# Kernel tuning notes

Hardware: AMD Instinct MI355X
Metric: run time of the kernel (lower is better)

Reference implementation:

```python
import jax, jax.numpy as jnp
import numpy as np

D = 2048      # token_dim (forced equal to visual feat dim by concat shapes)
V = 10000     # vocab size
B = 32        # batch
X = 36        # regions
T = 20        # max_len / caption length
FEAT = 2048


def setup_inputs() -> dict:
    key = jax.random.key(0)
    ks = jax.random.split(key, 20)
    s = 0.02
    inp = {
        "features": jax.random.normal(ks[0], (B, X, FEAT), jnp.float32),
        "caption": jax.random.randint(ks[1], (B, T), 0, V),
        "emb": jax.random.normal(ks[2], (V, D), jnp.float32) * s,
        # attention LSTMCell: input 3*D, hidden D
        "Wih_a": jax.random.normal(ks[3], (4 * D, 3 * D), jnp.float32) * s,
        "Whh_a": jax.random.normal(ks[4], (4 * D, D), jnp.float32) * s,
        "bih_a": jnp.zeros((4 * D,), jnp.float32),
        "bhh_a": jnp.zeros((4 * D,), jnp.float32),
        # language LSTMCell: input 2*D, hidden D
        "Wih_l": jax.random.normal(ks[5], (4 * D, 2 * D), jnp.float32) * s,
        "Whh_l": jax.random.normal(ks[6], (4 * D, D), jnp.float32) * s,
        "bih_l": jnp.zeros((4 * D,), jnp.float32),
        "bhh_l": jnp.zeros((4 * D,), jnp.float32),
        # attention MLP
        "Wv": jax.random.normal(ks[7], (D, FEAT), jnp.float32) * s,
        "bv": jnp.zeros((D,), jnp.float32),
        "Wh": jax.random.normal(ks[8], (D, D), jnp.float32) * s,
        "bh": jnp.zeros((D,), jnp.float32),
        "Wa": jax.random.normal(ks[9], (1, D), jnp.float32) * s,
        "ba": jnp.zeros((1,), jnp.float32),
        # output projection
        "Wfc": jax.random.normal(ks[10], (V, D), jnp.float32) * s,
        "bfc": jnp.zeros((V,), jnp.float32),
    }
    return inp


def _lstm_cell(x, h, c, Wih, Whh, bih, bhh):
    # PyTorch LSTMCell: gates in (i, f, g, o) order
    z = x @ Wih.T + bih + h @ Whh.T + bhh
    i, f, g, o = jnp.split(z, 4, axis=-1)
    c_new = jax.nn.sigmoid(f) * c + jax.nn.sigmoid(i) * jnp.tanh(g)
    h_new = jax.nn.sigmoid(o) * jnp.tanh(c_new)
    return h_new, c_new


def reference(features, caption, emb, Wih_a, Whh_a, bih_a, bhh_a,
              Wih_l, Whh_l, bih_l, bhh_l, Wv, bv, Wh, bh, Wa, ba, Wfc, bfc):
    v_bar = jnp.mean(features, axis=1)            # [B, 2048]
    embs = emb[caption]                            # [B, T, D]
    a_v = features @ Wv.T + bv                     # [B, X, D], t-invariant

    h0 = jnp.zeros((features.shape[0], D), features.dtype)
    carry0 = (h0, h0, h0, h0)  # (h_attn, c_attn, h_lang, c_lang)

    def step(carry, e_t):
        h_a, c_a, h_l, c_l = carry
        x = jnp.concatenate([h_l, v_bar, e_t], axis=1)          # [B, 3D]
        h_a, c_a = _lstm_cell(x, h_a, c_a, Wih_a, Whh_a, bih_a, bhh_a)
        # additive attention (NB: softmax over trailing singleton dim,
        # reproduced faithfully from the source -> weights are all ones)
        a_h = (h_a @ Wh.T + bh)[:, None, :]                      # [B, 1, D]
        a = jnp.tanh(a_v + a_h) @ Wa.T + ba                      # [B, X, 1]
        a_w = jax.nn.softmax(a, axis=-1)                         # [B, X, 1]
        v_hat = jnp.sum(a_w * features, axis=1)                  # [B, 2048]
        x2 = jnp.concatenate([h_a, v_hat], axis=1)               # [B, 2D]
        h_l, c_l = _lstm_cell(x2, h_l, c_l, Wih_l, Whh_l, bih_l, bhh_l)
        logits_t = h_l @ Wfc.T + bfc                             # [B, V]
        return (h_a, c_a, h_l, c_l), logits_t

    _, logits = jax.lax.scan(step, carry0, jnp.swapaxes(embs, 0, 1))  # [T, B, V]
    logits = jnp.swapaxes(logits, 0, 1)                               # [B, T, V]
    return jax.nn.log_softmax(logits, axis=2)
```

## Files before the change

kernel.cpp:

```cpp
#include <hip/hip_runtime.h>

typedef unsigned short u16;
typedef __attribute__((ext_vector_type(8))) short bf16x8;
typedef __attribute__((ext_vector_type(4))) float f32x4;

#define DD 2048
#define VV 10000
#define BB 32
#define TT 20

__device__ __forceinline__ u16 f2bf(float f) {
    unsigned u = __float_as_uint(f);
    u += 0x7fffu + ((u >> 16) & 1u);
    return (u16)(u >> 16);
}
__device__ __forceinline__ float bf2f(u16 h) {
    return __uint_as_float(((unsigned)h) << 16);
}

__global__ __launch_bounds__(256) void cast_weights(
    const float* __restrict__ Wih_a, const float* __restrict__ Whh_a,
    const float* __restrict__ Wih_l, const float* __restrict__ Whh_l,
    const float* __restrict__ Wfc,
    u16* __restrict__ Wcat_a, u16* __restrict__ Wcat_l, u16* __restrict__ Wfc_b)
{
    const long long S1 = 8192LL * 4096;
    const long long S3 = 20480000LL;
    long long g = (long long)blockIdx.x * 256 + threadIdx.x;
    long long e = g * 4;
    const float* src;
    u16* dst;
    if (e < S1) {
        int n = (int)(e >> 12), k = (int)(e & 4095);
        src = (k < 2048) ? (Wih_a + (size_t)n * 6144 + k)
                         : (Whh_a + (size_t)n * 2048 + (k - 2048));
        dst = Wcat_a + e;
    } else if (e < 2 * S1) {
        long long e2 = e - S1;
        int n = (int)(e2 >> 12), k = (int)(e2 & 4095);
        src = (k < 2048) ? (Wih_l + (size_t)n * 4096 + k)
                         : (Whh_l + (size_t)n * 2048 + (k - 2048));
        dst = Wcat_l + e2;
    } else {
        long long e3 = e - 2 * S1;
        if (e3 >= S3) return;
        src = Wfc + e3;
        dst = Wfc_b + e3;
    }
    float4 v = *(const float4*)src;
    ushort4 o;
    o.x = f2bf(v.x); o.y = f2bf(v.y); o.z = f2bf(v.z); o.w = f2bf(v.w);
    *(ushort4*)dst = o;
}

__global__ __launch_bounds__(256) void prep(
    const float* __restrict__ features,
    u16* __restrict__ vbar, u16* __restrict__ vhat,
    float* __restrict__ c_a, float* __restrict__ c_l,
    u16* __restrict__ Ha0, u16* __restrict__ Hl0)
{
    int i = blockIdx.x * 256 + threadIdx.x;
    int b = i >> 11, d = i & 2047;
    const float* f = features + (size_t)b * 36 * 2048 + d;
    float s = 0.f;
#pragma unroll
    for (int x = 0; x < 36; ++x) s += f[(size_t)x * 2048];
    vhat[i] = f2bf(s);
    vbar[i] = f2bf(s * (1.f / 36.f));
    c_a[i] = 0.f; c_l[i] = 0.f;
    Ha0[i] = 0;  Hl0[i] = 0;
}

__global__ __launch_bounds__(256) void embed_k(
    const float* __restrict__ emb, const int* __restrict__ caption,
    u16* __restrict__ embs)
{
    int i = blockIdx.x * 256 + threadIdx.x;
    int m = i >> 11, d = i & 2047;
    int t = m >> 5, b = m & 31;
    int tok = caption[b * TT + t];
    embs[i] = f2bf(emb[(size_t)tok * 2048 + d]);
}

template <int MT>
__global__ __launch_bounds__(256) void pre_gemm(
    const u16* __restrict__ A, const float* __restrict__ W,
    int ldw, int kofs,
    const float* __restrict__ bias0, const float* __restrict__ bias1,
    const float* __restrict__ addend, float* __restrict__ out)
{
    const int lane = threadIdx.x & 63;
    const int wv = threadIdx.x >> 6;
    const int lr = lane & 15, lq = lane >> 4;
    const int n0 = blockIdx.x * 64 + wv * 16;
    const int m0 = blockIdx.y * (MT * 16);

    f32x4 acc[MT];
#pragma unroll
    for (int i = 0; i < MT; ++i) acc[i] = (f32x4){0.f, 0.f, 0.f, 0.f};

    const float* wrow = W + (size_t)(n0 + lr) * ldw + kofs + lq * 8;
    const u16* arow = A + (size_t)(m0 + lr) * 2048 + lq * 8;

    for (int k = 0; k < 2048; k += 32) {
        float4 wlo = *(const float4*)(wrow + k);
        float4 whi = *(const float4*)(wrow + k + 4);
        bf16x8 bf;
        bf[0] = (short)f2bf(wlo.x); bf[1] = (short)f2bf(wlo.y);
        bf[2] = (short)f2bf(wlo.z); bf[3] = (short)f2bf(wlo.w);
        bf[4] = (short)f2bf(whi.x); bf[5] = (short)f2bf(whi.y);
        bf[6] = (short)f2bf(whi.z); bf[7] = (short)f2bf(whi.w);
#pragma unroll
        for (int mt = 0; mt < MT; ++mt) {
            bf16x8 af = *(const bf16x8*)(arow + (size_t)mt * 16 * 2048 + k);
            acc[mt] = __builtin_amdgcn_mfma_f32_16x16x32_bf16(af, bf, acc[mt], 0, 0, 0);
        }
    }
    const int n = n0 + lr;
    float badd = 0.f;
    if (bias0) badd += bias0[n];
    if (bias1) badd += bias1[n];
#pragma unroll
    for (int mt = 0; mt < MT; ++mt) {
#pragma unroll
        for (int r = 0; r < 4; ++r) {
            int m = m0 + mt * 16 + lq * 4 + r;
            float v = acc[mt][r] + badd;
            if (addend) v += addend[(size_t)(m & 31) * 8192 + n];
            out[(size_t)m * 8192 + n] = v;
        }
    }
}

__global__ __launch_bounds__(512) void step_kernel(
    const u16* __restrict__ A0, const u16* __restrict__ A1,
    const u16* __restrict__ W, const float* __restrict__ zconst,
    float* __restrict__ c, u16* __restrict__ hout)
{
    __shared__ float zred[4][32][64];
    const int lane = threadIdx.x & 63;
    const int w = threadIdx.x >> 6;
    const int lr = lane & 15, lq = lane >> 4;
    const int d0 = blockIdx.x * 16;

    const u16* Aptr = (w < 4) ? A0 : A1;
    const int kA = (w & 3) * 512 + lq * 8;
    const int kW = w * 512 + lq * 8;

    f32x4 acc[2][4];
#pragma unroll
    for (int m = 0; m < 2; ++m)
#pragma unroll
        for (int g = 0; g < 4; ++g) acc[m][g] = (f32x4){0.f, 0.f, 0.f, 0.f};

    const u16* a_row0 = Aptr + (size_t)lr * 2048 + kA;
    const u16* a_row1 = Aptr + (size_t)(16 + lr) * 2048 + kA;
    const u16* b_row[4];
#pragma unroll
    for (int g = 0; g < 4; ++g)
        b_row[g] = W + (size_t)(g * 2048 + d0 + lr) * 4096 + kW;

    for (int kk = 0; kk < 512; kk += 32) {
        bf16x8 a0 = *(const bf16x8*)(a_row0 + kk);
        bf16x8 a1 = *(const bf16x8*)(a_row1 + kk);
#pragma unroll
        for (int g = 0; g < 4; ++g) {
            bf16x8 bf = *(const bf16x8*)(b_row[g] + kk);
            acc[0][g] = __builtin_amdgcn_mfma_f32_16x16x32_bf16(a0, bf, acc[0][g], 0, 0, 0);
            acc[1][g] = __builtin_amdgcn_mfma_f32_16x16x32_bf16(a1, bf, acc[1][g], 0, 0, 0);
        }
    }

    if (w >= 4) {
#pragma unroll
        for (int m = 0; m < 2; ++m)
#pragma unroll
            for (int g = 0; g < 4; ++g)
#pragma unroll
                for (int r = 0; r < 4; ++r)
                    zred[w - 4][m * 16 + lq * 4 + r][g * 16 + lr] = acc[m][g][r];
    }
    __syncthreads();
    if (w < 4) {
#pragma unroll
        for (int m = 0; m < 2; ++m)
#pragma unroll
            for (int g = 0; g < 4; ++g)
#pragma unroll
                for (int r = 0; r < 4; ++r)
                    zred[w][m * 16 + lq * 4 + r][g * 16 + lr] += acc[m][g][r];
    }
    __syncthreads();

    const int b = threadIdx.x >> 4;
    const int j = threadIdx.x & 15;
    const int d = d0 + j;
    float z[4];
#pragma unroll
    for (int g = 0; g < 4; ++g) {
        float s = zconst[(size_t)b * 8192 + g * 2048 + d];
#pragma unroll
        for (int wv = 0; wv < 4; ++wv) s += zred[wv][b][g * 16 + j];
        z[g] = s;
    }
    float ig = 1.f / (1.f + __expf(-z[0]));
    float fg = 1.f / (1.f + __expf(-z[1]));
    float gg = tanhf(z[2]);
    float og = 1.f / (1.f + __expf(-z[3]));
    float cn = fg * c[(size_t)b * 2048 + d] + ig * gg;
    c[(size_t)b * 2048 + d] = cn;
    hout[(size_t)b * 2048 + d] = f2bf(og * tanhf(cn));
}

template <int MT>
__global__ __launch_bounds__(256) void logits_gemm(
    const u16* __restrict__ A, const u16* __restrict__ Wb,
    const float* __restrict__ bias, float* __restrict__ out)
{
    const int lane = threadIdx.x & 63;
    const int wv = threadIdx.x >> 6;
    const int lr = lane & 15, lq = lane >> 4;
    const int n0 = blockIdx.x * 64 + wv * 16;
    if (n0 >= VV) return;
    const int m0 = blockIdx.y * (MT * 16);

    f32x4 acc[MT];
#pragma unroll
    for (int i = 0; i < MT; ++i) acc[i] = (f32x4){0.f, 0.f, 0.f, 0.f};

    const u16* wrow = Wb + (size_t)(n0 + lr) * 2048 + lq * 8;
    const u16* arow = A + (size_t)(m0 + lr) * 2048 + lq * 8;

    for (int k = 0; k < 2048; k += 32) {
        bf16x8 bf = *(const bf16x8*)(wrow + k);
#pragma unroll
        for (int mt = 0; mt < MT; ++mt) {
            bf16x8 af = *(const bf16x8*)(arow + (size_t)mt * 16 * 2048 + k);
            acc[mt] = __builtin_amdgcn_mfma_f32_16x16x32_bf16(af, bf, acc[mt], 0, 0, 0);
        }
    }
    const int n = n0 + lr;
    const float bv = bias[n];
#pragma unroll
    for (int mt = 0; mt < MT; ++mt) {
#pragma unroll
        for (int r = 0; r < 4; ++r) {
            int m = m0 + mt * 16 + lq * 4 + r;
            int t = m >> 5, b = m & 31;
            out[(size_t)b * (TT * VV) + (size_t)t * VV + n] = acc[mt][r] + bv;
        }
    }
}

__global__ __launch_bounds__(256) void logsoftmax(float* __restrict__ out)
{
    float* p = out + (size_t)blockIdx.x * VV;
    const int tid = threadIdx.x, lane = tid & 63, wv = tid >> 6;
    __shared__ float red[4], red2[4];
    float mx = -1e30f;
    for (int i = tid; i < VV; i += 256) mx = fmaxf(mx, p[i]);
    for (int o = 32; o > 0; o >>= 1) mx = fmaxf(mx, __shfl_down(mx, o, 64));
    if (lane == 0) red[wv] = mx;
    __syncthreads();
    mx = fmaxf(fmaxf(red[0], red[1]), fmaxf(red[2], red[3]));
    float sum = 0.f;
    for (int i = tid; i < VV; i += 256) sum += __expf(p[i] - mx);
    for (int o = 32; o > 0; o >>= 1) sum += __shfl_down(sum, o, 64);
    if (lane == 0) red2[wv] = sum;
    __syncthreads();
    sum = red2[0] + red2[1] + red2[2] + red2[3];
    const float lse = mx + __logf(sum);
    for (int i = tid; i < VV; i += 256) p[i] = p[i] - lse;
}

extern "C" void kernel_launch(void* const* d_in, const int* in_sizes, int n_in,
                              void* d_out, int out_size, void* d_ws, size_t ws_size,
                              hipStream_t stream)
{
    const float* features = (const float*)d_in[0];
    const int*   caption  = (const int*)d_in[1];
    const float* emb      = (const float*)d_in[2];
    const float* Wih_a    = (const float*)d_in[3];
    const float* Whh_a    = (const float*)d_in[4];
    const float* bih_a    = (const float*)d_in[5];
    const float* bhh_a    = (const float*)d_in[6];
    const float* Wih_l    = (const float*)d_in[7];
    const float* Whh_l    = (const float*)d_in[8];
    const float* bih_l    = (const float*)d_in[9];
    const float* bhh_l    = (const float*)d_in[10];
    const float* Wfc      = (const float*)d_in[17];
    const float* bfc      = (const float*)d_in[18];
    float* out = (float*)d_out;

    char* ws = (char*)d_ws;
    size_t off = 0;
    auto alloc = [&](size_t bytes) { void* p = ws + off; off += (bytes + 255) & ~(size_t)255; return p; };
    u16* Wcat_a  = (u16*)alloc(8192ull * 4096 * 2);
    u16* Wcat_l  = (u16*)alloc(8192ull * 4096 * 2);
    u16* Wfc_b   = (u16*)alloc(10000ull * 2048 * 2);
    float* z_const = (float*)alloc(20ull * 32 * 8192 * 4);
    float* const_a = (float*)alloc(32ull * 8192 * 4);
    float* const_l = (float*)alloc(32ull * 8192 * 4);
    u16* embs    = (u16*)alloc(640ull * 2048 * 2);
    u16* vbar    = (u16*)alloc(32ull * 2048 * 2);
    u16* vhat    = (u16*)alloc(32ull * 2048 * 2);
    u16* Ha      = (u16*)alloc(2ull * 32 * 2048 * 2);
    u16* Hl      = (u16*)alloc(21ull * 32 * 2048 * 2);
    float* c_a   = (float*)alloc(32ull * 2048 * 4);
    float* c_l   = (float*)alloc(32ull * 2048 * 4);
    (void)ws_size; (void)in_sizes; (void)n_in; (void)out_size;

    cast_weights<<<dim3(85536), dim3(256), 0, stream>>>(
        Wih_a, Whh_a, Wih_l, Whh_l, Wfc, Wcat_a, Wcat_l, Wfc_b);
    prep<<<dim3(256), dim3(256), 0, stream>>>(features, vbar, vhat, c_a, c_l, Ha, Hl);
    embed_k<<<dim3(5120), dim3(256), 0, stream>>>(emb, caption, embs);
    pre_gemm<2><<<dim3(128, 1), dim3(256), 0, stream>>>(
        vbar, Wih_a, 6144, 2048, bih_a, bhh_a, nullptr, const_a);
    pre_gemm<2><<<dim3(128, 1), dim3(256), 0, stream>>>(
        vhat, Wih_l, 4096, 2048, bih_l, bhh_l, nullptr, const_l);
    pre_gemm<10><<<dim3(128, 4), dim3(256), 0, stream>>>(
        embs, Wih_a, 6144, 4096, nullptr, nullptr, const_a, z_const);

    for (int t = 0; t < 20; ++t) {
        u16* hl_prev = Hl + (size_t)t * 65536;
        u16* ha_prev = Ha + (size_t)(t & 1) * 65536;
        u16* ha_new  = Ha + (size_t)((t + 1) & 1) * 65536;
        u16* hl_new  = Hl + (size_t)(t + 1) * 65536;
        step_kernel<<<dim3(128), dim3(512), 0, stream>>>(
            hl_prev, ha_prev, Wcat_a, z_const + (size_t)t * 262144, c_a, ha_new);
        step_kernel<<<dim3(128), dim3(512), 0, stream>>>(
            ha_new, hl_prev, Wcat_l, const_l, c_l, hl_new);
    }

    logits_gemm<10><<<dim3(157, 4), dim3(256), 0, stream>>>(Hl + 65536, Wfc_b, bfc, out);
    logsoftmax<<<dim3(640), dim3(256), 0, stream>>>(out);
}
```

Measured before the change: 2.050 ms.

## Split step kernel across more blocks and software-prefetch GEMM operands

Result: no change. 2.085 ms (+1.7%).

```diff
diff --git a/kernel.cpp b/kernel.cpp
--- a/kernel.cpp
+++ b/kernel.cpp
@@ -102,19 +102,33 @@
     const float* wrow = W + (size_t)(n0 + lr) * ldw + kofs + lq * 8;
     const u16* arow = A + (size_t)(m0 + lr) * 2048 + lq * 8;
 
+    float4 wlon = *(const float4*)(wrow);
+    float4 whin = *(const float4*)(wrow + 4);
+    bf16x8 afn[MT];
+#pragma unroll
+    for (int mt = 0; mt < MT; ++mt)
+        afn[mt] = *(const bf16x8*)(arow + (size_t)mt * 16 * 2048);
+
     for (int k = 0; k < 2048; k += 32) {
-        float4 wlo = *(const float4*)(wrow + k);
-        float4 whi = *(const float4*)(wrow + k + 4);
+        float4 wlo = wlon, whi = whin;
+        bf16x8 afc[MT];
+#pragma unroll
+        for (int mt = 0; mt < MT; ++mt) afc[mt] = afn[mt];
+        if (k + 32 < 2048) {
+            wlon = *(const float4*)(wrow + k + 32);
+            whin = *(const float4*)(wrow + k + 36);
+#pragma unroll
+            for (int mt = 0; mt < MT; ++mt)
+                afn[mt] = *(const bf16x8*)(arow + (size_t)mt * 16 * 2048 + k + 32);
+        }
         bf16x8 bf;
         bf[0] = (short)f2bf(wlo.x); bf[1] = (short)f2bf(wlo.y);
         bf[2] = (short)f2bf(wlo.z); bf[3] = (short)f2bf(wlo.w);
         bf[4] = (short)f2bf(whi.x); bf[5] = (short)f2bf(whi.y);
         bf[6] = (short)f2bf(whi.z); bf[7] = (short)f2bf(whi.w);
 #pragma unroll
-        for (int mt = 0; mt < MT; ++mt) {
-            bf16x8 af = *(const bf16x8*)(arow + (size_t)mt * 16 * 2048 + k);
-            acc[mt] = __builtin_amdgcn_mfma_f32_16x16x32_bf16(af, bf, acc[mt], 0, 0, 0);
-        }
+        for (int mt = 0; mt < MT; ++mt)
+            acc[mt] = __builtin_amdgcn_mfma_f32_16x16x32_bf16(afc[mt], bf, acc[mt], 0, 0, 0);
     }
     const int n = n0 + lr;
     float badd = 0.f;
@@ -132,84 +146,73 @@
     }
 }
 
-__global__ __launch_bounds__(512) void step_kernel(
+__global__ __launch_bounds__(256) void step_kernel(
     const u16* __restrict__ A0, const u16* __restrict__ A1,
     const u16* __restrict__ W, const float* __restrict__ zconst,
     float* __restrict__ c, u16* __restrict__ hout)
 {
-    __shared__ float zred[4][32][64];
+    __shared__ float zred[4][32][16];
     const int lane = threadIdx.x & 63;
     const int w = threadIdx.x >> 6;
     const int lr = lane & 15, lq = lane >> 4;
-    const int d0 = blockIdx.x * 16;
-
-    const u16* Aptr = (w < 4) ? A0 : A1;
-    const int kA = (w & 3) * 512 + lq * 8;
-    const int kW = w * 512 + lq * 8;
-
-    f32x4 acc[2][4];
-#pragma unroll
-    for (int m = 0; m < 2; ++m)
-#pragma unroll
-        for (int g = 0; g < 4; ++g) acc[m][g] = (f32x4){0.f, 0.f, 0.f, 0.f};
+    const int d0 = blockIdx.x * 4;
+
+    const int g = lr >> 2, dd = lr & 3;
+    const int nrow = g * 2048 + d0 + dd;
+
+    const u16* Aptr = (w < 2) ? A0 : A1;
+    const int kA = (w & 1) * 1024 + lq * 8;
+    const int kW = w * 1024 + lq * 8;
+
+    f32x4 acc0 = (f32x4){0.f, 0.f, 0.f, 0.f};
+    f32x4 acc1 = (f32x4){0.f, 0.f, 0.f, 0.f};
 
     const u16* a_row0 = Aptr + (size_t)lr * 2048 + kA;
     const u16* a_row1 = Aptr + (size_t)(16 + lr) * 2048 + kA;
-    const u16* b_row[4];
-#pragma unroll
-    for (int g = 0; g < 4; ++g)
-        b_row[g] = W + (size_t)(g * 2048 + d0 + lr) * 4096 + kW;
-
-    for (int kk = 0; kk < 512; kk += 32) {
-        bf16x8 a0 = *(const bf16x8*)(a_row0 + kk);
-        bf16x8 a1 = *(const bf16x8*)(a_row1 + kk);
-#pragma unroll
-        for (int g = 0; g < 4; ++g) {
-            bf16x8 bf = *(const bf16x8*)(b_row[g] + kk);
-            acc[0][g] = __builtin_amdgcn_mfma_f32_16x16x32_bf16(a0, bf, acc[0][g], 0, 0, 0);
-            acc[1][g] = __builtin_amdgcn_mfma_f32_16x16x32_bf16(a1, bf, acc[1][g], 0, 0, 0);
-        }
-    }
-
-    if (w >= 4) {
-#pragma unroll
-        for (int m = 0; m < 2; ++m)
-#pragma unroll
-            for (int g = 0; g < 4; ++g)
-#pragma unroll
-                for (int r = 0; r < 4; ++r)
-                    zred[w - 4][m * 16 + lq * 4 + r][g * 16 + lr] = acc[m][g][r];
+    const u16* b_row  = W + (size_t)nrow * 4096 + kW;
+
+    bf16x8 a0n = *(const bf16x8*)(a_row0);
+    bf16x8 a1n = *(const bf16x8*)(a_row1);
+    bf16x8 bn  = *(const bf16x8*)(b_row);
+#pragma unroll
+    for (int kk = 0; kk < 1024; kk += 32) {
+        bf16x8 a0 = a0n, a1 = a1n, b = bn;
+        if (kk + 32 < 1024) {
+            a0n = *(const bf16x8*)(a_row0 + kk + 32);
+            a1n = *(const bf16x8*)(a_row1 + kk + 32);
+            bn  = *(const bf16x8*)(b_row  + kk + 32);
+        }
+        acc0 = __builtin_amdgcn_mfma_f32_16x16x32_bf16(a0, b, acc0, 0, 0, 0);
+        acc1 = __builtin_amdgcn_mfma_f32_16x16x32_bf16(a1, b, acc1, 0, 0, 0);
+    }
+
+#pragma unroll
+    for (int r = 0; r < 4; ++r) {
+        zred[w][lq * 4 + r][lr]      = acc0[r];
+        zred[w][16 + lq * 4 + r][lr] = acc1[r];
     }
     __syncthreads();
-    if (w < 4) {
-#pragma unroll
-        for (int m = 0; m < 2; ++m)
-#pragma unroll
-            for (int g = 0; g < 4; ++g)
-#pragma unroll
-                for (int r = 0; r < 4; ++r)
-                    zred[w][m * 16 + lq * 4 + r][g * 16 + lr] += acc[m][g][r];
-    }
-    __syncthreads();
-
-    const int b = threadIdx.x >> 4;
-    const int j = threadIdx.x & 15;
-    const int d = d0 + j;
-    float z[4];
-#pragma unroll
-    for (int g = 0; g < 4; ++g) {
-        float s = zconst[(size_t)b * 8192 + g * 2048 + d];
-#pragma unroll
-        for (int wv = 0; wv < 4; ++wv) s += zred[wv][b][g * 16 + j];
-        z[g] = s;
-    }
-    float ig = 1.f / (1.f + __expf(-z[0]));
-    float fg = 1.f / (1.f + __expf(-z[1]));
-    float gg = tanhf(z[2]);
-    float og = 1.f / (1.f + __expf(-z[3]));
-    float cn = fg * c[(size_t)b * 2048 + d] + ig * gg;
-    c[(size_t)b * 2048 + d] = cn;
-    hout[(size_t)b * 2048 + d] = f2bf(og * tanhf(cn));
+
+    if (threadIdx.x < 128) {
+        const int b = threadIdx.x >> 2;
+        const int j = threadIdx.x & 3;
+        const int d = d0 + j;
+        float z[4];
+#pragma unroll
+        for (int gg = 0; gg < 4; ++gg) {
+            float s = zconst[(size_t)b * 8192 + gg * 2048 + d];
+#pragma unroll
+            for (int wv = 0; wv < 4; ++wv) s += zred[wv][b][gg * 4 + j];
+            z[gg] = s;
+        }
+        float ig = 1.f / (1.f + __expf(-z[0]));
+        float fg = 1.f / (1.f + __expf(-z[1]));
+        float gv = tanhf(z[2]);
+        float og = 1.f / (1.f + __expf(-z[3]));
+        float cn = fg * c[(size_t)b * 2048 + d] + ig * gv;
+        c[(size_t)b * 2048 + d] = cn;
+        hout[(size_t)b * 2048 + d] = f2bf(og * tanhf(cn));
+    }
 }
 
 template <int MT>
@@ -231,13 +234,26 @@
     const u16* wrow = Wb + (size_t)(n0 + lr) * 2048 + lq * 8;
     const u16* arow = A + (size_t)(m0 + lr) * 2048 + lq * 8;
 
+    bf16x8 bfn = *(const bf16x8*)(wrow);
+    bf16x8 afn[MT];
+#pragma unroll
+    for (int mt = 0; mt < MT; ++mt)
+        afn[mt] = *(const bf16x8*)(arow + (size_t)mt * 16 * 2048);
+
     for (int k = 0; k < 2048; k += 32) {
-        bf16x8 bf = *(const bf16x8*)(wrow + k);
-#pragma unroll
-        for (int mt = 0; mt < MT; ++mt) {
-            bf16x8 af = *(const bf16x8*)(arow + (size_t)mt * 16 * 2048 + k);
-            acc[mt] = __builtin_amdgcn_mfma_f32_16x16x32_bf16(af, bf, acc[mt], 0, 0, 0);
-        }
+        bf16x8 bfc = bfn;
+        bf16x8 afc[MT];
+#pragma unroll
+        for (int mt = 0; mt < MT; ++mt) afc[mt] = afn[mt];
+        if (k + 32 < 2048) {
+            bfn = *(const bf16x8*)(wrow + k + 32);
+#pragma unroll
+            for (int mt = 0; mt < MT; ++mt)
+                afn[mt] = *(const bf16x8*)(arow + (size_t)mt * 16 * 2048 + k + 32);
+        }
+#pragma unroll
+        for (int mt = 0; mt < MT; ++mt)
+            acc[mt] = __builtin_amdgcn_mfma_f32_16x16x32_bf16(afc[mt], bfc, acc[mt], 0, 0, 0);
     }
     const int n = n0 + lr;
     const float bv = bias[n];
@@ -326,9 +342,9 @@
         u16* ha_prev = Ha + (size_t)(t & 1) * 65536;
         u16* ha_new  = Ha + (size_t)((t + 1) & 1) * 65536;
         u16* hl_new  = Hl + (size_t)(t + 1) * 65536;
-        step_kernel<<<dim3(128), dim3(512), 0, stream>>>(
+        step_kernel<<<dim3(512), dim3(256), 0, stream>>>(
             hl_prev, ha_prev, Wcat_a, z_const + (size_t)t * 262144, c_a, ha_new);
-        step_kernel<<<dim3(128), dim3(512), 0, stream>>>(
+        step_kernel<<<dim3(512), dim3(256), 0, stream>>>(
             ha_new, hl_prev, Wcat_l, const_l, c_l, hl_new);
     }
 
```

## Spread recurrent step over more blocks and retile large GEMMs

Applied to the files above, without the earlier changes.

Result: no change. 2.028 ms (-1.1%).

```diff
diff --git a/kernel.cpp b/kernel.cpp
--- a/kernel.cpp
+++ b/kernel.cpp
@@ -25,7 +25,7 @@
     u16* __restrict__ Wcat_a, u16* __restrict__ Wcat_l, u16* __restrict__ Wfc_b)
 {
     const long long S1 = 8192LL * 4096;
-    const long long S3 = 20480000LL;
+    const long long S3P = 10016LL * 2048;
     long long g = (long long)blockIdx.x * 256 + threadIdx.x;
     long long e = g * 4;
     const float* src;
@@ -43,9 +43,15 @@
         dst = Wcat_l + e2;
     } else {
         long long e3 = e - 2 * S1;
-        if (e3 >= S3) return;
+        if (e3 >= S3P) return;
+        dst = Wfc_b + e3;
+        int row = (int)(e3 >> 11);
+        if (row >= VV) {
+            ushort4 z; z.x = 0; z.y = 0; z.z = 0; z.w = 0;
+            *(ushort4*)dst = z;
+            return;
+        }
         src = Wfc + e3;
-        dst = Wfc_b + e3;
     }
     float4 v = *(const float4*)src;
     ushort4 o;
@@ -87,7 +93,7 @@
     const u16* __restrict__ A, const float* __restrict__ W,
     int ldw, int kofs,
     const float* __restrict__ bias0, const float* __restrict__ bias1,
-    const float* __restrict__ addend, float* __restrict__ out)
+    float* __restrict__ out)
 {
     const int lane = threadIdx.x & 63;
     const int wv = threadIdx.x >> 6;
@@ -125,9 +131,7 @@
 #pragma unroll
         for (int r = 0; r < 4; ++r) {
             int m = m0 + mt * 16 + lq * 4 + r;
-            float v = acc[mt][r] + badd;
-            if (addend) v += addend[(size_t)(m & 31) * 8192 + n];
-            out[(size_t)m * 8192 + n] = v;
+            out[(size_t)m * 8192 + n] = acc[mt][r] + badd;
         }
     }
 }
@@ -137,117 +141,162 @@
     const u16* __restrict__ W, const float* __restrict__ zconst,
     float* __restrict__ c, u16* __restrict__ hout)
 {
-    __shared__ float zred[4][32][64];
-    const int lane = threadIdx.x & 63;
-    const int w = threadIdx.x >> 6;
+    __shared__ float zred[8][32][17];
+    const int tid = threadIdx.x;
+    const int lane = tid & 63;
+    const int w = tid >> 6;
     const int lr = lane & 15, lq = lane >> 4;
-    const int d0 = blockIdx.x * 16;
+    const int d0 = blockIdx.x * 4;
+
+    const int g = lr >> 2, dd = lr & 3;
+    const int nrow = g * 2048 + d0 + dd;
 
     const u16* Aptr = (w < 4) ? A0 : A1;
     const int kA = (w & 3) * 512 + lq * 8;
-    const int kW = w * 512 + lq * 8;
-
-    f32x4 acc[2][4];
-#pragma unroll
-    for (int m = 0; m < 2; ++m)
-#pragma unroll
-        for (int g = 0; g < 4; ++g) acc[m][g] = (f32x4){0.f, 0.f, 0.f, 0.f};
-
-    const u16* a_row0 = Aptr + (size_t)lr * 2048 + kA;
-    const u16* a_row1 = Aptr + (size_t)(16 + lr) * 2048 + kA;
-    const u16* b_row[4];
-#pragma unroll
-    for (int g = 0; g < 4; ++g)
-        b_row[g] = W + (size_t)(g * 2048 + d0 + lr) * 4096 + kW;
-
-    for (int kk = 0; kk < 512; kk += 32) {
-        bf16x8 a0 = *(const bf16x8*)(a_row0 + kk);
-        bf16x8 a1 = *(const bf16x8*)(a_row1 + kk);
-#pragma unroll
-        for (int g = 0; g < 4; ++g) {
-            bf16x8 bf = *(const bf16x8*)(b_row[g] + kk);
-            acc[0][g] = __builtin_amdgcn_mfma_f32_16x16x32_bf16(a0, bf, acc[0][g], 0, 0, 0);
-            acc[1][g] = __builtin_amdgcn_mfma_f32_16x16x32_bf16(a1, bf, acc[1][g], 0, 0, 0);
-        }
-    }
-
-    if (w >= 4) {
-#pragma unroll
-        for (int m = 0; m < 2; ++m)
-#pragma unroll
-            for (int g = 0; g < 4; ++g)
-#pragma unroll
-                for (int r = 0; r < 4; ++r)
-                    zred[w - 4][m * 16 + lq * 4 + r][g * 16 + lr] = acc[m][g][r];
+
+    const u16* ar0 = Aptr + (size_t)lr * 2048 + kA;
+    const u16* ar1 = ar0 + 16 * 2048;
+    bf16x8 af0[16], af1[16];
+#pragma unroll
+    for (int kk = 0; kk < 16; ++kk) {
+        af0[kk] = *(const bf16x8*)(ar0 + kk * 32);
+        af1[kk] = *(const bf16x8*)(ar1 + kk * 32);
+    }
+
+    const u16* wrow = W + (size_t)nrow * 4096 + w * 512 + lq * 8;
+    f32x4 acc0 = (f32x4){0.f, 0.f, 0.f, 0.f};
+    f32x4 acc1 = (f32x4){0.f, 0.f, 0.f, 0.f};
+    bf16x8 wf[8];
+#pragma unroll
+    for (int kk = 0; kk < 8; ++kk)
+        wf[kk] = *(const bf16x8*)(wrow + kk * 32);
+#pragma unroll
+    for (int kk = 0; kk < 16; ++kk) {
+        acc0 = __builtin_amdgcn_mfma_f32_16x16x32_bf16(af0[kk], wf[kk & 7], acc0, 0, 0, 0);
+        acc1 = __builtin_amdgcn_mfma_f32_16x16x32_bf16(af1[kk], wf[kk & 7], acc1, 0, 0, 0);
+        if (kk < 8)
+            wf[kk] = *(const bf16x8*)(wrow + (kk + 8) * 32);
+    }
+
+#pragma unroll
+    for (int r = 0; r < 4; ++r) {
+        zred[w][lq * 4 + r][lr]      = acc0[r];
+        zred[w][16 + lq * 4 + r][lr] = acc1[r];
     }
     __syncthreads();
-    if (w < 4) {
-#pragma unroll
-        for (int m = 0; m < 2; ++m)
-#pragma unroll
-            for (int g = 0; g < 4; ++g)
-#pragma unroll
-                for (int r = 0; r < 4; ++r)
-                    zred[w][m * 16 + lq * 4 + r][g * 16 + lr] += acc[m][g][r];
-    }
-    __syncthreads();
-
-    const int b = threadIdx.x >> 4;
-    const int j = threadIdx.x & 15;
-    const int d = d0 + j;
-    float z[4];
-#pragma unroll
-    for (int g = 0; g < 4; ++g) {
-        float s = zconst[(size_t)b * 8192 + g * 2048 + d];
-#pragma unroll
-        for (int wv = 0; wv < 4; ++wv) s += zred[wv][b][g * 16 + j];
-        z[g] = s;
-    }
-    float ig = 1.f / (1.f + __expf(-z[0]));
-    float fg = 1.f / (1.f + __expf(-z[1]));
-    float gg = tanhf(z[2]);
-    float og = 1.f / (1.f + __expf(-z[3]));
-    float cn = fg * c[(size_t)b * 2048 + d] + ig * gg;
-    c[(size_t)b * 2048 + d] = cn;
-    hout[(size_t)b * 2048 + d] = f2bf(og * tanhf(cn));
-}
-
-template <int MT>
-__global__ __launch_bounds__(256) void logits_gemm(
-    const u16* __restrict__ A, const u16* __restrict__ Wb,
-    const float* __restrict__ bias, float* __restrict__ out)
-{
+
+    if (tid < 128) {
+        const int b = tid >> 2;
+        const int j = tid & 3;
+        const int d = d0 + j;
+        float z[4];
+#pragma unroll
+        for (int gg = 0; gg < 4; ++gg) {
+            float s = zconst[(size_t)b * 8192 + gg * 2048 + d];
+#pragma unroll
+            for (int wv = 0; wv < 8; ++wv) s += zred[wv][b][gg * 4 + j];
+            z[gg] = s;
+        }
+        float ig = 1.f / (1.f + __expf(-z[0]));
+        float fg = 1.f / (1.f + __expf(-z[1]));
+        float gv = tanhf(z[2]);
+        float og = 1.f / (1.f + __expf(-z[3]));
+        float cn = fg * c[(size_t)b * 2048 + d] + ig * gv;
+        c[(size_t)b * 2048 + d] = cn;
+        hout[(size_t)b * 2048 + d] = f2bf(og * tanhf(cn));
+    }
+}
+
+template <int MODE>
+__global__ __launch_bounds__(256) void big_gemm(
+    const u16* __restrict__ A, const void* __restrict__ Wp,
+    const float* __restrict__ extra, float* __restrict__ out)
+{
+    const int NWN = MODE ? 313 : 256;
+    const int nwg = MODE ? 783 : 640;
+    int bid = blockIdx.x;
+    {
+        int q = nwg >> 3, r = nwg & 7, x = bid & 7, o = bid >> 3;
+        bid = (x < r ? x * (q + 1) : r * (q + 1) + (x - r) * q) + o;
+    }
+    const int gw = bid * 4 + (int)(threadIdx.x >> 6);
+    const int wm = gw % 10;
+    const int wn = gw / 10;
+    if (wn >= NWN) return;
     const int lane = threadIdx.x & 63;
-    const int wv = threadIdx.x >> 6;
     const int lr = lane & 15, lq = lane >> 4;
-    const int n0 = blockIdx.x * 64 + wv * 16;
-    if (n0 >= VV) return;
-    const int m0 = blockIdx.y * (MT * 16);
-
-    f32x4 acc[MT];
-#pragma unroll
-    for (int i = 0; i < MT; ++i) acc[i] = (f32x4){0.f, 0.f, 0.f, 0.f};
-
-    const u16* wrow = Wb + (size_t)(n0 + lr) * 2048 + lq * 8;
+    const int m0 = wm * 64, n0 = wn * 32;
+
+    f32x4 acc[4][2];
+#pragma unroll
+    for (int mt = 0; mt < 4; ++mt)
+#pragma unroll
+        for (int nt = 0; nt < 2; ++nt) acc[mt][nt] = (f32x4){0.f, 0.f, 0.f, 0.f};
+
     const u16* arow = A + (size_t)(m0 + lr) * 2048 + lq * 8;
 
-    for (int k = 0; k < 2048; k += 32) {
-        bf16x8 bf = *(const bf16x8*)(wrow + k);
-#pragma unroll
-        for (int mt = 0; mt < MT; ++mt) {
-            bf16x8 af = *(const bf16x8*)(arow + (size_t)mt * 16 * 2048 + k);
-            acc[mt] = __builtin_amdgcn_mfma_f32_16x16x32_bf16(af, bf, acc[mt], 0, 0, 0);
-        }
-    }
-    const int n = n0 + lr;
-    const float bv = bias[n];
-#pragma unroll
-    for (int mt = 0; mt < MT; ++mt) {
-#pragma unroll
-        for (int r = 0; r < 4; ++r) {
-            int m = m0 + mt * 16 + lq * 4 + r;
-            int t = m >> 5, b = m & 31;
-            out[(size_t)b * (TT * VV) + (size_t)t * VV + n] = acc[mt][r] + bv;
+    if (MODE == 1) {
+        const u16* Wb = (const u16*)Wp;
+        const u16* wrow0 = Wb + (size_t)(n0 + lr) * 2048 + lq * 8;
+        const u16* wrow1 = wrow0 + 16 * 2048;
+#pragma unroll 2
+        for (int k = 0; k < 2048; k += 32) {
+            bf16x8 w0 = *(const bf16x8*)(wrow0 + k);
+            bf16x8 w1 = *(const bf16x8*)(wrow1 + k);
+#pragma unroll
+            for (int mt = 0; mt < 4; ++mt) {
+                bf16x8 a = *(const bf16x8*)(arow + (size_t)mt * 16 * 2048 + k);
+                acc[mt][0] = __builtin_amdgcn_mfma_f32_16x16x32_bf16(a, w0, acc[mt][0], 0, 0, 0);
+                acc[mt][1] = __builtin_amdgcn_mfma_f32_16x16x32_bf16(a, w1, acc[mt][1], 0, 0, 0);
+            }
+        }
+    } else {
+        const float* Wf = (const float*)Wp;
+        const float* wrow0 = Wf + (size_t)(n0 + lr) * 6144 + 4096 + lq * 8;
+        const float* wrow1 = wrow0 + (size_t)16 * 6144;
+#pragma unroll 2
+        for (int k = 0; k < 2048; k += 32) {
+            float4 p0 = *(const float4*)(wrow0 + k);
+            float4 p1 = *(const float4*)(wrow0 + k + 4);
+            float4 q0 = *(const float4*)(wrow1 + k);
+            float4 q1 = *(const float4*)(wrow1 + k + 4);
+            bf16x8 w0, w1;
+            w0[0] = (short)f2bf(p0.x); w0[1] = (short)f2bf(p0.y);
+            w0[2] = (short)f2bf(p0.z); w0[3] = (short)f2bf(p0.w);
+            w0[4] = (short)f2bf(p1.x); w0[5] = (short)f2bf(p1.y);
+            w0[6] = (short)f2bf(p1.z); w0[7] = (short)f2bf(p1.w);
+            w1[0] = (short)f2bf(q0.x); w1[1] = (short)f2bf(q0.y);
+            w1[2] = (short)f2bf(q0.z); w1[3] = (short)f2bf(q0.w);
+            w1[4] = (short)f2bf(q1.x); w1[5] = (short)f2bf(q1.y);
+            w1[6] = (short)f2bf(q1.z); w1[7] = (short)f2bf(q1.w);
+#pragma unroll
+            for (int mt = 0; mt < 4; ++mt) {
+                bf16x8 a = *(const bf16x8*)(arow + (size_t)mt * 16 * 2048 + k);
+                acc[mt][0] = __builtin_amdgcn_mfma_f32_16x16x32_bf16(a, w0, acc[mt][0], 0, 0, 0);
+                acc[mt][1] = __builtin_amdgcn_mfma_f32_16x16x32_bf16(a, w1, acc[mt][1], 0, 0, 0);
+            }
+        }
+    }
+
+#pragma unroll
+    for (int mt = 0; mt < 4; ++mt) {
+#pragma unroll
+        for (int nt = 0; nt < 2; ++nt) {
+            const int n = n0 + nt * 16 + lr;
+#pragma unroll
+            for (int r = 0; r < 4; ++r) {
+                const int m = m0 + mt * 16 + lq * 4 + r;
+                if (MODE == 0) {
+                    out[(size_t)m * 8192 + n] =
+                        acc[mt][nt][r] + extra[(size_t)(m & 31) * 8192 + n];
+                } else {
+                    if (n < VV) {
+                        const int t = m >> 5, b = m & 31;
+                        out[(size_t)b * (TT * VV) + (size_t)t * VV + n] =
+                            acc[mt][nt][r] + extra[n];
+                    }
+                }
+            }
         }
     }
 }
@@ -297,7 +346,7 @@
     auto alloc = [&](size_t bytes) { void* p = ws + off; off += (bytes + 255) & ~(size_t)255; return p; };
     u16* Wcat_a  = (u16*)alloc(8192ull * 4096 * 2);
     u16* Wcat_l  = (u16*)alloc(8192ull * 4096 * 2);
-    u16* Wfc_b   = (u16*)alloc(10000ull * 2048 * 2);
+    u16* Wfc_b   = (u16*)alloc(10016ull * 2048 * 2);
     float* z_const = (float*)alloc(20ull * 32 * 8192 * 4);
     float* const_a = (float*)alloc(32ull * 8192 * 4);
     float* const_l = (float*)alloc(32ull * 8192 * 4);
@@ -310,28 +359,29 @@
     float* c_l   = (float*)alloc(32ull * 2048 * 4);
     (void)ws_size; (void)in_sizes; (void)n_in; (void)out_size;
 
-    cast_weights<<<dim3(85536), dim3(256), 0, stream>>>(
+    cast_weights<<<dim3(85568), dim3(256), 0, stream>>>(
         Wih_a, Whh_a, Wih_l, Whh_l, Wfc, Wcat_a, Wcat_l, Wfc_b);
     prep<<<dim3(256), dim3(256), 0, stream>>>(features, vbar, vhat, c_a, c_l, Ha, Hl);
     embed_k<<<dim3(5120), dim3(256), 0, stream>>>(emb, caption, embs);
     pre_gemm<2><<<dim3(128, 1), dim3(256), 0, stream>>>(
-        vbar, Wih_a, 6144, 2048, bih_a, bhh_a, nullptr, const_a);
+        vbar, Wih_a, 6144, 2048, bih_a, bhh_a, const_a);
     pre_gemm<2><<<dim3(128, 1), dim3(256), 0, stream>>>(
-        vhat, Wih_l, 4096, 2048, bih_l, bhh_l, nullptr, const_l);
-    pre_gemm<10><<<dim3(128, 4), dim3(256), 0, stream>>>(
-        embs, Wih_a, 6144, 4096, nullptr, nullptr, const_a, z_const);
+        vhat, Wih_l, 4096, 2048, bih_l, bhh_l, const_l);
+    big_gemm<0><<<dim3(640), dim3(256), 0, stream>>>(
+        embs, (const void*)Wih_a, const_a, z_const);
 
     for (int t = 0; t < 20; ++t) {
         u16* hl_prev = Hl + (size_t)t * 65536;
         u16* ha_prev = Ha + (size_t)(t & 1) * 65536;
         u16* ha_new  = Ha + (size_t)((t + 1) & 1) * 65536;
         u16* hl_new  = Hl + (size_t)(t + 1) * 65536;
-        step_kernel<<<dim3(128), dim3(512), 0, stream>>>(
+        step_kernel<<<dim3(512), dim3(512), 0, stream>>>(
             hl_prev, ha_prev, Wcat_a, z_const + (size_t)t * 262144, c_a, ha_new);
-        step_kernel<<<dim3(128), dim3(512), 0, stream>>>(
+        step_kernel<<<dim3(512), dim3(512), 0, stream>>>(
             ha_new, hl_prev, Wcat_l, const_l, c_l, hl_new);
     }
 
-    logits_gemm<10><<<dim3(157, 4), dim3(256), 0, stream>>>(Hl + 65536, Wfc_b, bfc, out);
+    big_gemm<1><<<dim3(783), dim3(256), 0, stream>>>(
+        Hl + 65536, (const void*)Wfc_b, bfc, out);
     logsoftmax<<<dim3(640), dim3(256), 0, stream>>>(out);
 }
```
